# Kernel optimization log

Measured on AMD Instinct MI355X. Metric: run time of the kernel, lower is better.

Reference implementation:

```python
import jax, jax.numpy as jnp
import numpy as np

E = 262144   # number of half-edges / feature rows
C = 128      # in_channels
K = 4        # neighbors per half-edge
O = 256      # out_channels


def setup_inputs() -> dict:
    key = jax.random.key(0)
    k1, k2, k3, k4 = jax.random.split(key, 4)
    x = jax.random.normal(k1, (E, C), dtype=jnp.float32)
    neighbor_idx = jax.random.randint(k2, (E, K), 0, E, dtype=jnp.int64)
    W = jax.random.normal(k3, (K * C, O), dtype=jnp.float32) / np.sqrt(K * C)
    b = jax.random.normal(k4, (O,), dtype=jnp.float32) * 0.01
    return {"x": x, "neighbor_idx": neighbor_idx, "W": W, "b": b}


def reference(x, neighbor_idx, W, b):
    # gather neighbor features: [E, K, C] -> concat -> [E, K*C]
    gathered = x[neighbor_idx].reshape(x.shape[0], -1)
    # Linear + ReLU, batched over all half-edges
    out = jnp.maximum(gathered @ W + b, 0.0)
    return out
```

## Files before the change

### kernel.cpp

```cpp
#include <hip/hip_runtime.h>
#include <hip/hip_bf16.h>


#define E_ROWS 262144
#define C_IN   128
#define KN     4
#define KD     512
#define O_OUT  256
#define BM     128
#define BN     128
#define BK     32
#define NSTEPS 16
#define NTHREADS 512

typedef __attribute__((ext_vector_type(8))) short bf16x8;
typedef __attribute__((ext_vector_type(4))) float f32x4;

__device__ __forceinline__ unsigned short bf16_rne(float f) {
    unsigned u = __float_as_uint(f);
    return (unsigned short)((u + 0x7fffu + ((u >> 16) & 1u)) >> 16);
}

__global__ void prep_w(const float* __restrict__ W, uint4* __restrict__ wimg) {
    int cid = blockIdx.x * 256 + threadIdx.x;
    int cl  = cid & 511;
    int img = cid >> 9;
    int h   = img & 1;
    int s   = (img >> 1) & 15;
    int nb  = img >> 5;
    int nl  = cl >> 2;
    int cs  = cl & 3;
    int c   = cs ^ ((nl >> 1) & 3);
    int n   = nb * BN + nl;
    int kbase = s * BK + c * 8;
    unsigned short v[8];
    #pragma unroll
    for (int e = 0; e < 8; ++e) {
        float w = W[(size_t)(kbase + e) * O_OUT + n];
        unsigned u  = __float_as_uint(w);
        unsigned hb = (u + 0x7fffu + ((u >> 16) & 1u)) & 0xffff0000u;
        float r = w - __uint_as_float(hb);
        unsigned short lo = bf16_rne(r);
        unsigned short hi = (unsigned short)(hb >> 16);
        v[e] = h ? lo : hi;
    }
    uint4 o;
    o.x = (unsigned)v[0] | ((unsigned)v[1] << 16);
    o.y = (unsigned)v[2] | ((unsigned)v[3] << 16);
    o.z = (unsigned)v[4] | ((unsigned)v[5] << 16);
    o.w = (unsigned)v[6] | ((unsigned)v[7] << 16);
    wimg[cid] = o;
}

__global__ __launch_bounds__(NTHREADS, 4) void gemm(
    const float* __restrict__ x,
    const int* __restrict__ nidx,
    const uint4* __restrict__ wimg,
    const float* __restrict__ bias,
    float* __restrict__ out)
{
    __shared__ __align__(16) float A_s[BM * BK];
    __shared__ __align__(16) unsigned short B_s[2 * BN * BK];
    __shared__ int   idx_s[BM * KN];
    __shared__ float b_s[BN];

    const int t  = threadIdx.x;
    const int m0 = blockIdx.x * BM;
    const int nb = blockIdx.y;
    const int n0 = nb * BN;

    idx_s[t] = nidx[(size_t)m0 * KN + t];
    if (t < BN) b_s[t] = bias[n0 + t];

    const int l   = t & 63;
    const int wid = t >> 6;
    const int wm  = wid >> 1;
    const int wn  = wid & 1;
    const int lr  = l & 15;
    const int lg  = l >> 4;

    const int arow0 = t >> 3;
    const int ac0   = (t & 7) ^ (arow0 & 7);
    const int arow1 = (512 + t) >> 3;
    const int ac1   = ((512 + t) & 7) ^ (arow1 & 7);

    const uint4* wbase = wimg + (size_t)nb * (NSTEPS * 2 * 512);

    f32x4 acc[2][4];
    #pragma unroll
    for (int i = 0; i < 2; ++i)
        #pragma unroll
        for (int jj = 0; jj < 4; ++jj)
            acc[i][jj] = (f32x4){0.f, 0.f, 0.f, 0.f};

    char* Abase = (char*)&A_s[0];
    char* Bbase = (char*)&B_s[0];

    __syncthreads();

    #pragma unroll 1
    for (int s = 0; s < NSTEPS; ++s) {
        const int j  = s >> 2;
        const int kc = (s & 3) << 5;

        {
            const float* srcA0 = x + (size_t)idx_s[arow0 * KN + j] * C_IN + kc + (ac0 << 2);
            const float* srcA1 = x + (size_t)idx_s[arow1 * KN + j] * C_IN + kc + (ac1 << 2);
            __builtin_amdgcn_global_load_lds(
                (const __attribute__((address_space(1))) void*)srcA0,
                (__attribute__((address_space(3))) void*)(Abase + (wid << 10)), 16, 0, 0);
            __builtin_amdgcn_global_load_lds(
                (const __attribute__((address_space(1))) void*)srcA1,
                (__attribute__((address_space(3))) void*)(Abase + 8192 + (wid << 10)), 16, 0, 0);
        }
        {
            const uint4* srcB0 = wbase + (size_t)(s * 2 + 0) * 512 + t;
            const uint4* srcB1 = wbase + (size_t)(s * 2 + 1) * 512 + t;
            __builtin_amdgcn_global_load_lds(
                (const __attribute__((address_space(1))) void*)srcB0,
                (__attribute__((address_space(3))) void*)(Bbase + (wid << 10)), 16, 0, 0);
            __builtin_amdgcn_global_load_lds(
                (const __attribute__((address_space(1))) void*)srcB1,
                (__attribute__((address_space(3))) void*)(Bbase + 8192 + (wid << 10)), 16, 0, 0);
        }
        __syncthreads();

        bf16x8 bh[4], bl[4];
        #pragma unroll
        for (int nf = 0; nf < 4; ++nf) {
            int nl  = (wn << 6) + (nf << 4) + lr;
            int cB  = lg ^ ((nl >> 1) & 3);
            int off = nl * 64 + cB * 16;
            bh[nf] = *(const bf16x8*)(Bbase + off);
            bl[nf] = *(const bf16x8*)(Bbase + 8192 + off);
        }

        #pragma unroll
        for (int mf = 0; mf < 2; ++mf) {
            int row = (wm << 5) + (mf << 4) + lr;
            int c0  = (2 * lg)     ^ (row & 7);
            int c1  = (2 * lg + 1) ^ (row & 7);
            f32x4 a0 = *(const f32x4*)(Abase + row * 128 + c0 * 16);
            f32x4 a1 = *(const f32x4*)(Abase + row * 128 + c1 * 16);
            float av[8];
            av[0]=a0[0]; av[1]=a0[1]; av[2]=a0[2]; av[3]=a0[3];
            av[4]=a1[0]; av[5]=a1[1]; av[6]=a1[2]; av[7]=a1[3];
            bf16x8 ah, al;
            #pragma unroll
            for (int e = 0; e < 8; ++e) {
                unsigned u  = __float_as_uint(av[e]);
                unsigned hb = u & 0xffff0000u;
                ah[e] = (short)(u >> 16);
                al[e] = (short)bf16_rne(av[e] - __uint_as_float(hb));
            }
            #pragma unroll
            for (int nf = 0; nf < 4; ++nf) {
                acc[mf][nf] = __builtin_amdgcn_mfma_f32_16x16x32_bf16(ah, bh[nf], acc[mf][nf], 0, 0, 0);
                acc[mf][nf] = __builtin_amdgcn_mfma_f32_16x16x32_bf16(ah, bl[nf], acc[mf][nf], 0, 0, 0);
                acc[mf][nf] = __builtin_amdgcn_mfma_f32_16x16x32_bf16(al, bh[nf], acc[mf][nf], 0, 0, 0);
            }
        }
        __syncthreads();
    }

    #pragma unroll
    for (int mf = 0; mf < 2; ++mf) {
        #pragma unroll
        for (int nf = 0; nf < 4; ++nf) {
            int colL = (wn << 6) + (nf << 4) + lr;
            int col  = n0 + colL;
            float bv = b_s[colL];
            int rowb = m0 + (wm << 5) + (mf << 4) + (lg << 2);
            #pragma unroll
            for (int r = 0; r < 4; ++r) {
                float v = acc[mf][nf][r] + bv;
                out[(size_t)(rowb + r) * O_OUT + col] = fmaxf(v, 0.f);
            }
        }
    }
}

extern "C" void kernel_launch(void* const* d_in, const int* in_sizes, int n_in,
                              void* d_out, int out_size, void* d_ws, size_t ws_size,
                              hipStream_t stream) {
    const float* x    = (const float*)d_in[0];
    const int*   nidx = (const int*)d_in[1];
    const float* W    = (const float*)d_in[2];
    const float* bias = (const float*)d_in[3];
    float* out  = (float*)d_out;
    uint4* wimg = (uint4*)d_ws;

    hipLaunchKernelGGL(prep_w, dim3(128), dim3(256), 0, stream, W, wimg);
    hipLaunchKernelGGL(gemm, dim3(E_ROWS / BM, O_OUT / BN), dim3(NTHREADS), 0, stream,
                       x, nidx, wimg, bias, out);
}
```

Baseline: 542.3 us.

## Halve GEMM block to 256 threads with larger per-warp tiles; stage W prep through LDS

The gather-GEMM kernel now runs 256 threads per block instead of 512. Each wave computes a 64x64 output tile (4x4 MFMA fragments) instead of 32x64, and each thread issues four A gather loads and four B loads per k-step. This cuts barrier participants and raises per-wave MFMA work and B-fragment reuse, at the cost of more accumulator registers and fewer waves to hide gather latency. The weight-prep kernel now loads one k-slab of W into shared memory with coalesced float4 reads before building the split-bf16 image, instead of doing strided column reads from global memory.

```diff
diff --git a/kernel.cpp b/kernel.cpp
--- a/kernel.cpp
+++ b/kernel.cpp
@@ -5,13 +5,12 @@
 #define E_ROWS 262144
 #define C_IN   128
 #define KN     4
-#define KD     512
 #define O_OUT  256
 #define BM     128
 #define BN     128
 #define BK     32
 #define NSTEPS 16
-#define NTHREADS 512
+#define NT     256
 
 typedef __attribute__((ext_vector_type(8))) short bf16x8;
 typedef __attribute__((ext_vector_type(4))) float f32x4;
@@ -22,37 +21,48 @@
 }
 
 __global__ void prep_w(const float* __restrict__ W, uint4* __restrict__ wimg) {
-    int cid = blockIdx.x * 256 + threadIdx.x;
-    int cl  = cid & 511;
-    int img = cid >> 9;
-    int h   = img & 1;
-    int s   = (img >> 1) & 15;
-    int nb  = img >> 5;
-    int nl  = cl >> 2;
-    int cs  = cl & 3;
-    int c   = cs ^ ((nl >> 1) & 3);
-    int n   = nb * BN + nl;
-    int kbase = s * BK + c * 8;
-    unsigned short v[8];
-    #pragma unroll
-    for (int e = 0; e < 8; ++e) {
-        float w = W[(size_t)(kbase + e) * O_OUT + n];
-        unsigned u  = __float_as_uint(w);
-        unsigned hb = (u + 0x7fffu + ((u >> 16) & 1u)) & 0xffff0000u;
-        float r = w - __uint_as_float(hb);
-        unsigned short lo = bf16_rne(r);
-        unsigned short hi = (unsigned short)(hb >> 16);
-        v[e] = h ? lo : hi;
-    }
-    uint4 o;
-    o.x = (unsigned)v[0] | ((unsigned)v[1] << 16);
-    o.y = (unsigned)v[2] | ((unsigned)v[3] << 16);
-    o.z = (unsigned)v[4] | ((unsigned)v[5] << 16);
-    o.w = (unsigned)v[6] | ((unsigned)v[7] << 16);
-    wimg[cid] = o;
-}
-
-__global__ __launch_bounds__(NTHREADS, 4) void gemm(
+    __shared__ float Ws[32][260];
+    const int s = blockIdx.x;
+    const int t = threadIdx.x;
+    #pragma unroll
+    for (int i = 0; i < 8; ++i) {
+        int v4 = i * 256 + t;
+        int k  = v4 >> 6;
+        int n4 = v4 & 63;
+        float4 w = ((const float4*)W)[(size_t)(s * 32 + k) * 64 + n4];
+        *(float4*)&Ws[k][n4 * 4] = w;
+    }
+    __syncthreads();
+    #pragma unroll
+    for (int i = 0; i < 8; ++i) {
+        int q  = i * 256 + t;
+        int nb = q >> 10;
+        int h  = (q >> 9) & 1;
+        int cl = q & 511;
+        int nl = cl >> 2;
+        int cs = cl & 3;
+        int c  = cs ^ ((nl >> 1) & 3);
+        int n  = nb * 128 + nl;
+        int kb = c * 8;
+        unsigned short v[8];
+        #pragma unroll
+        for (int e = 0; e < 8; ++e) {
+            float w = Ws[kb + e][n];
+            unsigned u  = __float_as_uint(w);
+            unsigned hb = (u + 0x7fffu + ((u >> 16) & 1u)) & 0xffff0000u;
+            float r = w - __uint_as_float(hb);
+            v[e] = h ? bf16_rne(r) : (unsigned short)(hb >> 16);
+        }
+        uint4 o;
+        o.x = (unsigned)v[0] | ((unsigned)v[1] << 16);
+        o.y = (unsigned)v[2] | ((unsigned)v[3] << 16);
+        o.z = (unsigned)v[4] | ((unsigned)v[5] << 16);
+        o.w = (unsigned)v[6] | ((unsigned)v[7] << 16);
+        wimg[(size_t)nb * 16384 + (size_t)(2 * s + h) * 512 + cl] = o;
+    }
+}
+
+__global__ __launch_bounds__(NT, 4) void gemm(
     const float* __restrict__ x,
     const int* __restrict__ nidx,
     const uint4* __restrict__ wimg,
@@ -69,7 +79,8 @@
     const int nb = blockIdx.y;
     const int n0 = nb * BN;
 
-    idx_s[t] = nidx[(size_t)m0 * KN + t];
+    idx_s[t]       = nidx[(size_t)m0 * KN + t];
+    idx_s[t + 256] = nidx[(size_t)m0 * KN + 256 + t];
     if (t < BN) b_s[t] = bias[n0 + t];
 
     const int l   = t & 63;
@@ -79,16 +90,19 @@
     const int lr  = l & 15;
     const int lg  = l >> 4;
 
-    const int arow0 = t >> 3;
-    const int ac0   = (t & 7) ^ (arow0 & 7);
-    const int arow1 = (512 + t) >> 3;
-    const int ac1   = ((512 + t) & 7) ^ (arow1 & 7);
-
-    const uint4* wbase = wimg + (size_t)nb * (NSTEPS * 2 * 512);
-
-    f32x4 acc[2][4];
-    #pragma unroll
-    for (int i = 0; i < 2; ++i)
+    int arow[4], ac[4];
+    #pragma unroll
+    for (int i = 0; i < 4; ++i) {
+        int q   = t + 256 * i;
+        arow[i] = q >> 3;
+        ac[i]   = (q & 7) ^ (arow[i] & 7);
+    }
+
+    const uint4* wbase = wimg + (size_t)nb * 16384;
+
+    f32x4 acc[4][4];
+    #pragma unroll
+    for (int i = 0; i < 4; ++i)
         #pragma unroll
         for (int jj = 0; jj < 4; ++jj)
             acc[i][jj] = (f32x4){0.f, 0.f, 0.f, 0.f};
@@ -103,25 +117,26 @@
         const int j  = s >> 2;
         const int kc = (s & 3) << 5;
 
-        {
-            const float* srcA0 = x + (size_t)idx_s[arow0 * KN + j] * C_IN + kc + (ac0 << 2);
-            const float* srcA1 = x + (size_t)idx_s[arow1 * KN + j] * C_IN + kc + (ac1 << 2);
+        #pragma unroll
+        for (int i = 0; i < 4; ++i) {
+            const float* src = x + (size_t)idx_s[arow[i] * KN + j] * C_IN + kc + (ac[i] << 2);
             __builtin_amdgcn_global_load_lds(
-                (const __attribute__((address_space(1))) void*)srcA0,
-                (__attribute__((address_space(3))) void*)(Abase + (wid << 10)), 16, 0, 0);
+                (const __attribute__((address_space(1))) void*)src,
+                (__attribute__((address_space(3))) void*)(Abase + (i << 12) + (wid << 10)),
+                16, 0, 0);
+        }
+        #pragma unroll
+        for (int i = 0; i < 2; ++i) {
+            const uint4* srcH = wbase + (size_t)(2 * s) * 512 + (t + 256 * i);
+            const uint4* srcL = wbase + (size_t)(2 * s + 1) * 512 + (t + 256 * i);
             __builtin_amdgcn_global_load_lds(
-                (const __attribute__((address_space(1))) void*)srcA1,
-                (__attribute__((address_space(3))) void*)(Abase + 8192 + (wid << 10)), 16, 0, 0);
-        }
-        {
-            const uint4* srcB0 = wbase + (size_t)(s * 2 + 0) * 512 + t;
-            const uint4* srcB1 = wbase + (size_t)(s * 2 + 1) * 512 + t;
+                (const __attribute__((address_space(1))) void*)srcH,
+                (__attribute__((address_space(3))) void*)(Bbase + (i << 12) + (wid << 10)),
+                16, 0, 0);
             __builtin_amdgcn_global_load_lds(
-                (const __attribute__((address_space(1))) void*)srcB0,
-                (__attribute__((address_space(3))) void*)(Bbase + (wid << 10)), 16, 0, 0);
-            __builtin_amdgcn_global_load_lds(
-                (const __attribute__((address_space(1))) void*)srcB1,
-                (__attribute__((address_space(3))) void*)(Bbase + 8192 + (wid << 10)), 16, 0, 0);
+                (const __attribute__((address_space(1))) void*)srcL,
+                (__attribute__((address_space(3))) void*)(Bbase + 8192 + (i << 12) + (wid << 10)),
+                16, 0, 0);
         }
         __syncthreads();
 
@@ -136,12 +151,11 @@
         }
 
         #pragma unroll
-        for (int mf = 0; mf < 2; ++mf) {
-            int row = (wm << 5) + (mf << 4) + lr;
-            int c0  = (2 * lg)     ^ (row & 7);
-            int c1  = (2 * lg + 1) ^ (row & 7);
+        for (int mf = 0; mf < 4; ++mf) {
+            int row = (wm << 6) + (mf << 4) + lr;
+            int c0  = (lg << 1) ^ (lr & 7);
             f32x4 a0 = *(const f32x4*)(Abase + row * 128 + c0 * 16);
-            f32x4 a1 = *(const f32x4*)(Abase + row * 128 + c1 * 16);
+            f32x4 a1 = *(const f32x4*)(Abase + row * 128 + (c0 ^ 1) * 16);
             float av[8];
             av[0]=a0[0]; av[1]=a0[1]; av[2]=a0[2]; av[3]=a0[3];
             av[4]=a1[0]; av[5]=a1[1]; av[6]=a1[2]; av[7]=a1[3];
@@ -164,13 +178,13 @@
     }
 
     #pragma unroll
-    for (int mf = 0; mf < 2; ++mf) {
+    for (int mf = 0; mf < 4; ++mf) {
         #pragma unroll
         for (int nf = 0; nf < 4; ++nf) {
             int colL = (wn << 6) + (nf << 4) + lr;
             int col  = n0 + colL;
             float bv = b_s[colL];
-            int rowb = m0 + (wm << 5) + (mf << 4) + (lg << 2);
+            int rowb = m0 + (wm << 6) + (mf << 4) + (lg << 2);
             #pragma unroll
             for (int r = 0; r < 4; ++r) {
                 float v = acc[mf][nf][r] + bv;
@@ -190,7 +204,7 @@
     float* out  = (float*)d_out;
     uint4* wimg = (uint4*)d_ws;
 
-    hipLaunchKernelGGL(prep_w, dim3(128), dim3(256), 0, stream, W, wimg);
-    hipLaunchKernelGGL(gemm, dim3(E_ROWS / BM, O_OUT / BN), dim3(NTHREADS), 0, stream,
+    hipLaunchKernelGGL(prep_w, dim3(NSTEPS), dim3(256), 0, stream, W, wimg);
+    hipLaunchKernelGGL(gemm, dim3(E_ROWS / BM, O_OUT / BN), dim3(NT), 0, stream,
                        x, nidx, wimg, bias, out);
 }
```

After: 610.6 us. +12.6%, slower.
